# Kernel optimization log

Measured on AMD Instinct MI355X. Metric: run time of the kernel, lower is better.

Reference implementation:

```python
import jax, jax.numpy as jnp
import numpy as np

DZ = 64
DC = 32
T = 2_000_000


def setup_inputs() -> dict:
    key = jax.random.key(0)
    k1, k2 = jax.random.split(key)
    Z = jax.random.normal(k1, (T, DZ), dtype=jnp.float32)
    # beta = rand(dc, dz) * 0.01, matching nn.Parameter init
    beta = jax.random.uniform(k2, (DC, DZ), dtype=jnp.float32) * 0.01
    return {"Z": Z, "beta": beta}


def reference(Z, beta):
    # Batched version of the per-timestep loop:
    #   norm_t = 1 + sum(exp(beta[:-1] @ Z[t]))
    #   probs[t, :-1] = exp(beta[:-1] @ Z[t]) / norm_t ; probs[t, -1] = 1 / norm_t
    dc = beta.shape[0]
    logits = jnp.einsum('td,cd->tc', Z, beta[:-1])        # (T, dc-1)
    e = jnp.exp(logits)                                   # unshifted exp, as in original
    norm = 1.0 + jnp.sum(e, axis=-1, keepdims=True)       # (T, 1)
    probs = jnp.concatenate([e / norm, 1.0 / norm], axis=-1)  # (T, dc)
    most_likely = jnp.argmax(probs, axis=-1)              # (T,)
    cats = jax.nn.one_hot(most_likely, dc, dtype=Z.dtype)  # (T, dc)
    return cats
```

## Files before the change

kernel.cpp:

```cpp
#include <hip/hip_runtime.h>
#include <math.h>


constexpr int DZ = 64;
constexpr int DC = 32;
constexpr int NC = 31;
constexpr int BLOCK = 256;

__global__ __launch_bounds__(BLOCK) void decoder_cat_kernel(
    const float* __restrict__ Z, const float* __restrict__ beta,
    float* __restrict__ out, int T)
{
    const int tid  = threadIdx.x;
    const int row  = blockIdx.x * BLOCK + tid;
    const bool live = (row < T);

    float4 z[16];
    if (live) {
        const float4* zp = (const float4*)(Z + (size_t)row * DZ);
#pragma unroll
        for (int i = 0; i < 16; ++i) z[i] = zp[i];
    } else {
#pragma unroll
        for (int i = 0; i < 16; ++i) z[i] = make_float4(0.f, 0.f, 0.f, 0.f);
    }

    float acc[NC];
#pragma unroll
    for (int c = 0; c < NC; ++c) acc[c] = 0.0f;

#pragma unroll
    for (int d4 = 0; d4 < 16; ++d4) {
        const float4 z4 = z[d4];
#pragma unroll
        for (int c = 0; c < NC; ++c) {
            const float* b = beta + c * DZ + d4 * 4;
            acc[c] = fmaf(b[3], z4.w,
                     fmaf(b[2], z4.z,
                     fmaf(b[1], z4.y,
                     fmaf(b[0], z4.x, acc[c]))));
        }
    }

    float s = 1.0f;
#pragma unroll
    for (int c = 0; c < NC; ++c) { acc[c] = expf(acc[c]); s += acc[c]; }

    float best = -1.0f;
    int   bidx = 0;
#pragma unroll
    for (int c = 0; c < NC; ++c) {
        float p = acc[c] / s;
        if (p > best) { best = p; bidx = c; }
    }
    if (1.0f / s > best) bidx = NC;

    const int lane  = tid & 63;
    const int wrow0 = blockIdx.x * BLOCK + (tid & ~63);
#pragma unroll
    for (int k = 0; k < 8; ++k) {
        int cid = lane + 64 * k;
        int r   = cid >> 3;
        int c4  = cid & 7;
        int widx = __shfl(bidx, r, 64);
        int grow = wrow0 + r;
        if (grow < T) {
            float4 v;
            v.x = (c4 * 4 + 0 == widx) ? 1.0f : 0.0f;
            v.y = (c4 * 4 + 1 == widx) ? 1.0f : 0.0f;
            v.z = (c4 * 4 + 2 == widx) ? 1.0f : 0.0f;
            v.w = (c4 * 4 + 3 == widx) ? 1.0f : 0.0f;
            *(float4*)(out + (size_t)grow * DC + c4 * 4) = v;
        }
    }
}

extern "C" void kernel_launch(void* const* d_in, const int* in_sizes, int n_in,
                              void* d_out, int out_size, void* d_ws, size_t ws_size,
                              hipStream_t stream)
{
    const float* Z    = (const float*)d_in[0];
    const float* beta = (const float*)d_in[1];
    float* out        = (float*)d_out;
    const int T = in_sizes[0] / DZ;
    const int grid = (T + BLOCK - 1) / BLOCK;
    hipLaunchKernelGGL(decoder_cat_kernel, dim3(grid), dim3(BLOCK), 0, stream,
                       Z, beta, out, T);
}
```

Measured before the change: 741.9 us.

## Stage Z rows through LDS with coalesced wave loads and XOR swizzle

Each wave now loads its 64 rows of Z cooperatively: 8 lanes cover one 128-byte half row, so global reads are contiguous rather than one 256-byte row per thread. The data goes through per-wave shared memory with an XOR swizzle to avoid bank conflicts. It is processed in two halves, with the second half's global loads issued before computing on the first. This adds LDS traffic, 32 KB of shared memory per block that may limit occupancy, and wave-level barriers.

```diff
diff --git a/kernel.cpp b/kernel.cpp
--- a/kernel.cpp
+++ b/kernel.cpp
@@ -6,41 +6,84 @@
 constexpr int DC = 32;
 constexpr int NC = 31;
 constexpr int BLOCK = 256;
+constexpr int WAVES = BLOCK / 64;
 
 __global__ __launch_bounds__(BLOCK) void decoder_cat_kernel(
     const float* __restrict__ Z, const float* __restrict__ beta,
     float* __restrict__ out, int T)
 {
     const int tid  = threadIdx.x;
-    const int row  = blockIdx.x * BLOCK + tid;
-    const bool live = (row < T);
+    const int lane = tid & 63;
+    const int wave = tid >> 6;
+    const int wrow0 = blockIdx.x * BLOCK + (tid & ~63);
 
-    float4 z[16];
-    if (live) {
-        const float4* zp = (const float4*)(Z + (size_t)row * DZ);
-#pragma unroll
-        for (int i = 0; i < 16; ++i) z[i] = zp[i];
-    } else {
-#pragma unroll
-        for (int i = 0; i < 16; ++i) z[i] = make_float4(0.f, 0.f, 0.f, 0.f);
-    }
+    __shared__ float lds[WAVES][2048];
+    float* __restrict__ wl = lds[wave];
+
+    const int subrow = lane >> 3;
+    const int sc     = lane & 7;
+    const int wbase  = subrow * 32 + ((sc ^ subrow) * 4);
+    float* const rb  = wl + lane * 32;
+
+    const bool full = (wrow0 + 64) <= T;
 
     float acc[NC];
 #pragma unroll
     for (int c = 0; c < NC; ++c) acc[c] = 0.0f;
 
+    const float* gb = Z + (size_t)(wrow0 + subrow) * DZ + sc * 4;
+
+    float4 g0[8];
+    if (full) {
 #pragma unroll
-    for (int d4 = 0; d4 < 16; ++d4) {
-        const float4 z4 = z[d4];
+        for (int j = 0; j < 8; ++j) g0[j] = *(const float4*)(gb + j * (8 * DZ));
+    } else {
 #pragma unroll
-        for (int c = 0; c < NC; ++c) {
-            const float* b = beta + c * DZ + d4 * 4;
-            acc[c] = fmaf(b[3], z4.w,
-                     fmaf(b[2], z4.z,
-                     fmaf(b[1], z4.y,
-                     fmaf(b[0], z4.x, acc[c]))));
+        for (int j = 0; j < 8; ++j) {
+            int r = wrow0 + subrow + 8 * j; r = (r < T) ? r : (T - 1);
+            g0[j] = *(const float4*)(Z + (size_t)r * DZ + sc * 4);
         }
     }
+#pragma unroll
+    for (int j = 0; j < 8; ++j) *(float4*)(wl + j * 256 + wbase) = g0[j];
+
+    float4 g1[8];
+    if (full) {
+#pragma unroll
+        for (int j = 0; j < 8; ++j) g1[j] = *(const float4*)(gb + 32 + j * (8 * DZ));
+    } else {
+#pragma unroll
+        for (int j = 0; j < 8; ++j) {
+            int r = wrow0 + subrow + 8 * j; r = (r < T) ? r : (T - 1);
+            g1[j] = *(const float4*)(Z + (size_t)r * DZ + 32 + sc * 4);
+        }
+    }
+    __builtin_amdgcn_wave_barrier();
+
+    auto consume_half = [&](int hbase) {
+#pragma unroll
+        for (int c = 0; c < 8; ++c) {
+            const float4 z4 = *(const float4*)(rb + ((c ^ sc) * 4));
+            const int d4 = hbase + c;
+#pragma unroll
+            for (int cat = 0; cat < NC; ++cat) {
+                const float* b = beta + cat * DZ + d4 * 4;
+                acc[cat] = fmaf(b[3], z4.w,
+                           fmaf(b[2], z4.z,
+                           fmaf(b[1], z4.y,
+                           fmaf(b[0], z4.x, acc[cat]))));
+            }
+        }
+    };
+
+    consume_half(0);
+    __builtin_amdgcn_wave_barrier();
+
+#pragma unroll
+    for (int j = 0; j < 8; ++j) *(float4*)(wl + j * 256 + wbase) = g1[j];
+    __builtin_amdgcn_wave_barrier();
+
+    consume_half(8);
 
     float s = 1.0f;
 #pragma unroll
@@ -55,8 +98,6 @@
     }
     if (1.0f / s > best) bidx = NC;
 
-    const int lane  = tid & 63;
-    const int wrow0 = blockIdx.x * BLOCK + (tid & ~63);
 #pragma unroll
     for (int k = 0; k < 8; ++k) {
         int cid = lane + 64 * k;
```

Measured after the change: 818.0 us. 10.3% more time.
